# Kernel tuning notes

Measured on AMD Instinct MI355X. Metric: run time of the kernel, lower is better.

## Reference

```python
import jax, jax.numpy as jnp
import numpy as np

SEQ, IN, H = 65536, 64, 128


def setup_inputs() -> dict:
    key = jax.random.key(0)
    ks = jax.random.split(key, 7)
    s_i, s_h = 1.0 / np.sqrt(IN), 1.0 / np.sqrt(H)
    return {
        "input_seq": jax.random.normal(ks[0], (SEQ, IN), jnp.float32),
        "W_ih": jax.random.normal(ks[1], (4 * H, IN), jnp.float32) * s_i,
        "W_hh": jax.random.normal(ks[2], (4 * H, H), jnp.float32) * s_h,
        "b_ih": jax.random.normal(ks[3], (4 * H,), jnp.float32) * s_h,
        "b_hh": jax.random.normal(ks[4], (4 * H,), jnp.float32) * s_h,
        "W_lin": jax.random.normal(ks[5], (1, H), jnp.float32) * s_h,
        "b_lin": jax.random.normal(ks[6], (1,), jnp.float32) * s_h,
    }


def reference(input_seq, W_ih, W_hh, b_ih, b_hh, W_lin, b_lin):
    # Precompute input contributions to all gates: [SEQ, 4H]
    x_gates = input_seq @ W_ih.T + b_ih + b_hh

    def step(carry, xg):
        h, c = carry
        gates = xg + h @ W_hh.T  # [4H]
        i, f, g, o = jnp.split(gates, 4)
        i = jax.nn.sigmoid(i)
        f = jax.nn.sigmoid(f)
        g = jnp.tanh(g)
        o = jax.nn.sigmoid(o)
        c = f * c + i * g
        h = o * jnp.tanh(c)
        return (h, c), None

    h0 = jnp.zeros((H,), input_seq.dtype)
    c0 = jnp.zeros((H,), input_seq.dtype)
    (hT, _), _ = jax.lax.scan(step, (h0, c0), x_gates)
    # outputs[-1] == sigmoid(linear(h_T)); shape [1]
    return jax.nn.sigmoid(hT @ W_lin.T + b_lin)
```

## Files before the change

### kernel.cpp

```cpp
#include <hip/hip_runtime.h>

#define SEQ 65536
#define IN_DIM 64
#define H 128
#define G4 512

typedef _Float16 half_t;
typedef half_t half2_t __attribute__((ext_vector_type(2)));
typedef half_t half8_t __attribute__((ext_vector_type(8)));

__device__ __forceinline__ float fast_rcp(float x) { return __builtin_amdgcn_rcpf(x); }

__device__ __forceinline__ float sigmoid_f(float x) {
    x = fminf(fmaxf(x, -30.f), 30.f);
    return fast_rcp(1.f + __expf(-x));
}

__device__ __forceinline__ float tanh_f(float x) {
    x = fminf(fmaxf(x, -15.f), 15.f);
    float e = __expf(2.f * x);
    return (e - 1.f) * fast_rcp(e + 1.f);
}

#if __has_builtin(__builtin_amdgcn_fdot2)
__device__ __forceinline__ float dot2(half2_t a, half2_t b, float c) {
    return __builtin_amdgcn_fdot2(a, b, c, false);
}
#else
__device__ __forceinline__ float dot2(half2_t a, half2_t b, float c) {
    return c + (float)a[0] * (float)b[0] + (float)a[1] * (float)b[1];
}
#endif

__device__ __forceinline__ half2_t pick2(half8_t v, int i0) {
    half2_t r; r[0] = v[i0]; r[1] = v[i0 + 1]; return r;
}

__device__ __forceinline__ half8_t cvt8(const float* p) {
    float4 a = *(const float4*)p;
    float4 b = *(const float4*)(p + 4);
    half8_t r;
    r[0] = (half_t)a.x; r[1] = (half_t)a.y; r[2] = (half_t)a.z; r[3] = (half_t)a.w;
    r[4] = (half_t)b.x; r[5] = (half_t)b.y; r[6] = (half_t)b.z; r[7] = (half_t)b.w;
    return r;
}

#if __has_builtin(__builtin_amdgcn_mov_dpp)
__device__ __forceinline__ float qx1(float x) {
    return __int_as_float(__builtin_amdgcn_mov_dpp(__float_as_int(x), 0xB1, 0xF, 0xF, true));
}
__device__ __forceinline__ float qx2(float x) {
    return __int_as_float(__builtin_amdgcn_mov_dpp(__float_as_int(x), 0x4E, 0xF, 0xF, true));
}
#else
__device__ __forceinline__ float qx1(float x) { return __shfl_xor(x, 1, 4); }
__device__ __forceinline__ float qx2(float x) { return __shfl_xor(x, 2, 4); }
#endif

__global__ __launch_bounds__(256) void xg_gemm(
    const float* __restrict__ x, const float* __restrict__ Wih,
    const float* __restrict__ bih, const float* __restrict__ bhh,
    float* __restrict__ xg)
{
    long long gid = (long long)blockIdx.x * 256 + threadIdx.x;
    int s = (int)(gid >> 9);
    int rr = (int)(gid & 511);
    int j = rr >> 2, g = rr & 3;
    int row = g * H + j;
    const float* xr = x + (long long)s * IN_DIM;
    const float* wr = Wih + (long long)row * IN_DIM;
    float a0 = 0.f, a1 = 0.f, a2 = 0.f, a3 = 0.f;
#pragma unroll
    for (int k = 0; k < IN_DIM; k += 4) {
        float4 iv = *(const float4*)(xr + k);
        float4 wv = *(const float4*)(wr + k);
        a0 += wv.x * iv.x; a1 += wv.y * iv.y;
        a2 += wv.z * iv.z; a3 += wv.w * iv.w;
    }
    xg[gid] = (a0 + a1) + (a2 + a3) + bih[row] + bhh[row];
}

__global__ __launch_bounds__(256, 1) void lstm_scan(
    const float* __restrict__ Whh, const float* __restrict__ Wlin,
    const float* __restrict__ blin, const float* __restrict__ xg,
    float* __restrict__ out)
{
    __shared__ __align__(16) half_t shbuf[2][H];
    const int tid = threadIdx.x;
    const int ql = tid & 3;
    const int j0 = (tid >> 2) * 2;
    const int c0 = ql * 32;
    const int jrow = j0 + (ql & 1);

#define LOADW(P, ROW)                                                     \
    half8_t P##0 = cvt8(Whh + (size_t)(ROW) * H + c0 + 0),                \
            P##1 = cvt8(Whh + (size_t)(ROW) * H + c0 + 8),                \
            P##2 = cvt8(Whh + (size_t)(ROW) * H + c0 + 16),               \
            P##3 = cvt8(Whh + (size_t)(ROW) * H + c0 + 24);
    LOADW(wi0, j0)           LOADW(wi1, j0 + 1)
    LOADW(wf0, 128 + j0)     LOADW(wf1, 129 + j0)
    LOADW(wg0, 256 + j0)     LOADW(wg1, 257 + j0)
    LOADW(wo0, 384 + j0)     LOADW(wo1, 385 + j0)
#undef LOADW
#define PIN(A, B, C, D) asm volatile("" : "+v"(A), "+v"(B), "+v"(C), "+v"(D))
    PIN(wi00, wi01, wi02, wi03); PIN(wi10, wi11, wi12, wi13);
    PIN(wf00, wf01, wf02, wf03); PIN(wf10, wf11, wf12, wf13);
    PIN(wg00, wg01, wg02, wg03); PIN(wg10, wg11, wg12, wg13);
    PIN(wo00, wo01, wo02, wo03); PIN(wo10, wo11, wo12, wo13);
#undef PIN

    float c = 0.f;
    float4 xgv = {0.f, 0.f, 0.f, 0.f};
    if (ql < 2) xgv = *(const float4*)(xg + (size_t)jrow * 4);
    if (tid < H) shbuf[0][tid] = (half_t)0.f;
    __syncthreads();

#define DOT8(ACC, WV, HV)                                                 \
    ACC = dot2(pick2(WV, 0), pick2(HV, 0), ACC);                          \
    ACC = dot2(pick2(WV, 2), pick2(HV, 2), ACC);                          \
    ACC = dot2(pick2(WV, 4), pick2(HV, 4), ACC);                          \
    ACC = dot2(pick2(WV, 6), pick2(HV, 6), ACC);
#define DOTROW(ACC, P)                                                    \
    DOT8(ACC, P##0, h0) DOT8(ACC, P##1, h1)                               \
    DOT8(ACC, P##2, h2) DOT8(ACC, P##3, h3)
#define QRED(X) X += qx1(X); X += qx2(X);

#define STEP(RB, WB, T)                                                   \
    {                                                                     \
        const half8_t* hp = (const half8_t*)&shbuf[RB][c0];               \
        half8_t h0 = hp[0], h1 = hp[1], h2 = hp[2], h3 = hp[3];           \
        int tn = (T) + 1; if (tn > SEQ - 1) tn = SEQ - 1;                 \
        float4 xg_n = {0.f, 0.f, 0.f, 0.f};                               \
        if (ql < 2)                                                       \
            xg_n = *(const float4*)(xg + (size_t)tn * G4 + jrow * 4);     \
        float ai0 = 0.f, ai1 = 0.f, af0 = 0.f, af1 = 0.f;                 \
        float ag0 = 0.f, ag1 = 0.f, ao0 = 0.f, ao1 = 0.f;                 \
        DOTROW(ai0, wi0) DOTROW(ai1, wi1)                                 \
        DOTROW(af0, wf0) DOTROW(af1, wf1)                                 \
        DOTROW(ag0, wg0) DOTROW(ag1, wg1)                                 \
        DOTROW(ao0, wo0) DOTROW(ao1, wo1)                                 \
        QRED(ai0) QRED(ai1) QRED(af0) QRED(af1)                           \
        QRED(ag0) QRED(ag1) QRED(ao0) QRED(ao1)                           \
        if (ql < 2) {                                                     \
            float si = ql ? ai1 : ai0, sf = ql ? af1 : af0;               \
            float sg = ql ? ag1 : ag0, so = ql ? ao1 : ao0;               \
            float gi = sigmoid_f(si + xgv.x);                             \
            float gf = sigmoid_f(sf + xgv.y);                             \
            float gg = tanh_f(sg + xgv.z);                                \
            float go = sigmoid_f(so + xgv.w);                             \
            c = gf * c + gi * gg;                                         \
            shbuf[WB][jrow] = (half_t)(go * tanh_f(c));                   \
        }                                                                 \
        __syncthreads();                                                  \
        xgv = xg_n;                                                       \
    }

    for (int t = 0; t < SEQ; t += 2) {
        STEP(0, 1, t)
        STEP(1, 0, t + 1)
    }
#undef STEP
#undef QRED
#undef DOTROW
#undef DOT8

    if (tid < 64) {
        float p = (float)shbuf[0][tid] * Wlin[tid] +
                  (float)shbuf[0][tid + 64] * Wlin[tid + 64];
#pragma unroll
        for (int off = 32; off > 0; off >>= 1) p += __shfl_down(p, off);
        if (tid == 0) out[0] = sigmoid_f(p + blin[0]);
    }
}

__global__ __launch_bounds__(512, 2) void lstm_scan_fb(
    const float* __restrict__ x, const float* __restrict__ Wih,
    const float* __restrict__ Whh, const float* __restrict__ bih,
    const float* __restrict__ bhh, const float* __restrict__ Wlin,
    const float* __restrict__ blin, float* __restrict__ out)
{
    __shared__ __align__(16) half_t sh_h[H];
    __shared__ __align__(16) float  sh_g[G4];
    const int row = threadIdx.x;
    const float* wrow = Whh + (long long)row * H;

    half8_t w0  = cvt8(wrow + 0),   w1  = cvt8(wrow + 8);
    half8_t w2  = cvt8(wrow + 16),  w3  = cvt8(wrow + 24);
    half8_t w4  = cvt8(wrow + 32),  w5  = cvt8(wrow + 40);
    half8_t w6  = cvt8(wrow + 48),  w7  = cvt8(wrow + 56);
    half8_t w8  = cvt8(wrow + 64),  w9  = cvt8(wrow + 72);
    half8_t w10 = cvt8(wrow + 80),  w11 = cvt8(wrow + 88);
    half8_t w12 = cvt8(wrow + 96),  w13 = cvt8(wrow + 104);
    half8_t w14 = cvt8(wrow + 112), w15 = cvt8(wrow + 120);

    const float bsum = bih[row] + bhh[row];
    float c = 0.f;
    if (row < H) sh_h[row] = (half_t)0.f;

    float xg_cur;
    {
        float a = bsum;
        const float* wir = Wih + (long long)row * IN_DIM;
#pragma unroll
        for (int k = 0; k < IN_DIM; k += 4) {
            float4 iv = *(const float4*)(x + k);
            float4 wv = *(const float4*)(wir + k);
            a += wv.x * iv.x + wv.y * iv.y + wv.z * iv.z + wv.w * iv.w;
        }
        xg_cur = a;
    }
    const bool is_g = (row >= 2 * H) && (row < 3 * H);
    __syncthreads();

    const half8_t* hch = (const half8_t*)sh_h;

    for (int t = 0; t < SEQ; ++t) {
        float xg_nxt = 0.f;
        if (t + 1 < SEQ) {
            const float* xr = x + (size_t)(t + 1) * IN_DIM;
            const float* wir = Wih + (long long)row * IN_DIM;
            float a = bsum;
#pragma unroll
            for (int k = 0; k < IN_DIM; k += 4) {
                float4 iv = *(const float4*)(xr + k);
                float4 wv = *(const float4*)(wir + k);
                a += wv.x * iv.x + wv.y * iv.y + wv.z * iv.z + wv.w * iv.w;
            }
            xg_nxt = a;
        }
        float a0 = 0.f, a1 = 0.f, a2 = 0.f, a3 = 0.f;
#define DOTC(WV, CI)                                                     \
        {   half8_t hv = hch[CI];                                        \
            a0 = dot2(pick2(WV, 0), pick2(hv, 0), a0);                   \
            a1 = dot2(pick2(WV, 2), pick2(hv, 2), a1);                   \
            a2 = dot2(pick2(WV, 4), pick2(hv, 4), a2);                   \
            a3 = dot2(pick2(WV, 6), pick2(hv, 6), a3); }
        DOTC(w0, 0)  DOTC(w1, 1)  DOTC(w2, 2)   DOTC(w3, 3)
        DOTC(w4, 4)  DOTC(w5, 5)  DOTC(w6, 6)   DOTC(w7, 7)
        DOTC(w8, 8)  DOTC(w9, 9)  DOTC(w10, 10) DOTC(w11, 11)
        DOTC(w12, 12) DOTC(w13, 13) DOTC(w14, 14) DOTC(w15, 15)
#undef DOTC
        float pre = xg_cur + ((a0 + a1) + (a2 + a3));
        float gv = is_g ? tanh_f(pre) : sigmoid_f(pre);
        sh_g[row] = gv;
        __syncthreads();
        if (row >= 3 * H) {
            int j = row - 3 * H;
            float ig = sh_g[j];
            float fg = sh_g[H + j];
            float gg = sh_g[2 * H + j];
            c = fg * c + ig * gg;
            sh_h[j] = (half_t)(gv * tanh_f(c));
        }
        __syncthreads();
        xg_cur = xg_nxt;
    }

    if (row < 64) {
        float p = (float)sh_h[row] * Wlin[row] +
                  (float)sh_h[row + 64] * Wlin[row + 64];
#pragma unroll
        for (int off = 32; off > 0; off >>= 1) p += __shfl_down(p, off);
        if (row == 0) out[0] = sigmoid_f(p + blin[0]);
    }
}

extern "C" void kernel_launch(void* const* d_in, const int* in_sizes, int n_in,
                              void* d_out, int out_size, void* d_ws, size_t ws_size,
                              hipStream_t stream)
{
    const float* x    = (const float*)d_in[0];
    const float* Wih  = (const float*)d_in[1];
    const float* Whh  = (const float*)d_in[2];
    const float* bih  = (const float*)d_in[3];
    const float* bhh  = (const float*)d_in[4];
    const float* Wlin = (const float*)d_in[5];
    const float* blin = (const float*)d_in[6];
    float* out = (float*)d_out;

    const size_t need = (size_t)SEQ * G4 * sizeof(float);
    if (ws_size >= need) {
        float* xg = (float*)d_ws;
        xg_gemm<<<(SEQ * G4) / 256, 256, 0, stream>>>(x, Wih, bih, bhh, xg);
        lstm_scan<<<1, 256, 0, stream>>>(Whh, Wlin, blin, xg, out);
    } else {
        lstm_scan_fb<<<1, 512, 0, stream>>>(x, Wih, Whh, bih, bhh, Wlin,
                                            blin, out);
    }
}
```

Baseline: 33.12 ms.

## Spread gate activations across quad lanes and exchange via DPP in LSTM scan

Each lane of a 4-lane quad now computes the activation for one gate type (i, f, g, o) for two hidden units, and the four results are exchanged with DPP permutes, so all quad lanes do activation work instead of only half of them. tanh is computed as 2*sigmoid(2x)-1 so every lane runs the same instruction sequence. The xg buffer goes back to its natural row layout, loaded as float2 and prefetched two steps ahead. The __syncthreads is replaced with an explicit lgkmcnt wait, s_barrier and a sched_barrier. The aim is a shorter serial critical path per timestep, at the cost of extra permutes and reliance on hand-placed barrier semantics.

```diff
diff --git a/kernel.cpp b/kernel.cpp
--- a/kernel.cpp
+++ b/kernel.cpp
@@ -14,12 +14,6 @@
 __device__ __forceinline__ float sigmoid_f(float x) {
     x = fminf(fmaxf(x, -30.f), 30.f);
     return fast_rcp(1.f + __expf(-x));
-}
-
-__device__ __forceinline__ float tanh_f(float x) {
-    x = fminf(fmaxf(x, -15.f), 15.f);
-    float e = __expf(2.f * x);
-    return (e - 1.f) * fast_rcp(e + 1.f);
 }
 
 #if __has_builtin(__builtin_amdgcn_fdot2)
@@ -45,17 +39,14 @@
     return r;
 }
 
-#if __has_builtin(__builtin_amdgcn_mov_dpp)
-__device__ __forceinline__ float qx1(float x) {
-    return __int_as_float(__builtin_amdgcn_mov_dpp(__float_as_int(x), 0xB1, 0xF, 0xF, true));
-}
-__device__ __forceinline__ float qx2(float x) {
-    return __int_as_float(__builtin_amdgcn_mov_dpp(__float_as_int(x), 0x4E, 0xF, 0xF, true));
-}
-#else
-__device__ __forceinline__ float qx1(float x) { return __shfl_xor(x, 1, 4); }
-__device__ __forceinline__ float qx2(float x) { return __shfl_xor(x, 2, 4); }
-#endif
+template <int CTRL>
+__device__ __forceinline__ float qperm(float x) {
+    return __int_as_float(
+        __builtin_amdgcn_mov_dpp(__float_as_int(x), CTRL, 0xF, 0xF, true));
+}
+#define qx1(x)  qperm<0xB1>(x)
+#define qx2(x)  qperm<0x4E>(x)
+#define qrev(x) qperm<0x1B>(x)
 
 __global__ __launch_bounds__(256) void xg_gemm(
     const float* __restrict__ x, const float* __restrict__ Wih,
@@ -64,11 +55,9 @@
 {
     long long gid = (long long)blockIdx.x * 256 + threadIdx.x;
     int s = (int)(gid >> 9);
-    int rr = (int)(gid & 511);
-    int j = rr >> 2, g = rr & 3;
-    int row = g * H + j;
+    int r = (int)(gid & 511);
     const float* xr = x + (long long)s * IN_DIM;
-    const float* wr = Wih + (long long)row * IN_DIM;
+    const float* wr = Wih + (long long)r * IN_DIM;
     float a0 = 0.f, a1 = 0.f, a2 = 0.f, a3 = 0.f;
 #pragma unroll
     for (int k = 0; k < IN_DIM; k += 4) {
@@ -77,7 +66,7 @@
         a0 += wv.x * iv.x; a1 += wv.y * iv.y;
         a2 += wv.z * iv.z; a3 += wv.w * iv.w;
     }
-    xg[gid] = (a0 + a1) + (a2 + a3) + bih[row] + bhh[row];
+    xg[gid] = (a0 + a1) + (a2 + a3) + bih[r] + bhh[r];
 }
 
 __global__ __launch_bounds__(256, 1) void lstm_scan(
@@ -90,7 +79,6 @@
     const int ql = tid & 3;
     const int j0 = (tid >> 2) * 2;
     const int c0 = ql * 32;
-    const int jrow = j0 + (ql & 1);
 
 #define LOADW(P, ROW)                                                     \
     half8_t P##0 = cvt8(Whh + (size_t)(ROW) * H + c0 + 0),                \
@@ -109,9 +97,14 @@
     PIN(wo00, wo01, wo02, wo03); PIN(wo10, wo11, wo12, wo13);
 #undef PIN
 
+    const bool isg = (ql == 2);
+    const bool l0  = (ql == 0);
+    const float* xgbase = xg + ql * H + j0;
     float c = 0.f;
-    float4 xgv = {0.f, 0.f, 0.f, 0.f};
-    if (ql < 2) xgv = *(const float4*)(xg + (size_t)jrow * 4);
+
+    float2 xg_c = *(const float2*)(xgbase + (size_t)0 * G4);
+    float2 xg_n = *(const float2*)(xgbase + (size_t)1 * G4);
+
     if (tid < H) shbuf[0][tid] = (half_t)0.f;
     __syncthreads();
 
@@ -129,10 +122,8 @@
     {                                                                     \
         const half8_t* hp = (const half8_t*)&shbuf[RB][c0];               \
         half8_t h0 = hp[0], h1 = hp[1], h2 = hp[2], h3 = hp[3];           \
-        int tn = (T) + 1; if (tn > SEQ - 1) tn = SEQ - 1;                 \
-        float4 xg_n = {0.f, 0.f, 0.f, 0.f};                               \
-        if (ql < 2)                                                       \
-            xg_n = *(const float4*)(xg + (size_t)tn * G4 + jrow * 4);     \
+        int tp = (T) + 2; if (tp > SEQ - 1) tp = SEQ - 1;                 \
+        float2 xg_p = *(const float2*)(xgbase + (size_t)tp * G4);         \
         float ai0 = 0.f, ai1 = 0.f, af0 = 0.f, af1 = 0.f;                 \
         float ag0 = 0.f, ag1 = 0.f, ao0 = 0.f, ao1 = 0.f;                 \
         DOTROW(ai0, wi0) DOTROW(ai1, wi1)                                 \
@@ -141,18 +132,33 @@
         DOTROW(ao0, wo0) DOTROW(ao1, wo1)                                 \
         QRED(ai0) QRED(ai1) QRED(af0) QRED(af1)                           \
         QRED(ag0) QRED(ag1) QRED(ao0) QRED(ao1)                           \
-        if (ql < 2) {                                                     \
-            float si = ql ? ai1 : ai0, sf = ql ? af1 : af0;               \
-            float sg = ql ? ag1 : ag0, so = ql ? ao1 : ao0;               \
-            float gi = sigmoid_f(si + xgv.x);                             \
-            float gf = sigmoid_f(sf + xgv.y);                             \
-            float gg = tanh_f(sg + xgv.z);                                \
-            float go = sigmoid_f(so + xgv.w);                             \
-            c = gf * c + gi * gg;                                         \
-            shbuf[WB][jrow] = (half_t)(go * tanh_f(c));                   \
-        }                                                                 \
-        __syncthreads();                                                  \
-        xgv = xg_n;                                                       \
+                         \
+        float sa = ai0, sb = ai1;                                         \
+        if (ql == 1) { sa = af0; sb = af1; }                              \
+        if (ql == 2) { sa = ag0; sb = ag1; }                              \
+        if (ql == 3) { sa = ao0; sb = ao1; }                              \
+        float xa = sa + xg_c.x, xb = sb + xg_c.y;                         \
+        float ua = isg ? xa + xa : xa;                                    \
+        float ub = isg ? xb + xb : xb;                                    \
+        float ra = sigmoid_f(ua), rb = sigmoid_f(ub);                     \
+        float gva = isg ? ra + ra - 1.f : ra;        \
+        float gvb = isg ? rb + rb - 1.f : rb;                             \
+          \
+        float fA = qx1(gva), iB = qx1(gvb);                               \
+        float gA = qx2(gva), oB = qx2(gvb);                               \
+        float oA = qrev(gva), gB = qrev(gvb);                             \
+        float ii = l0 ? gva : iB;                                         \
+        float ff = l0 ? fA  : gvb;                                        \
+        float gg = l0 ? gA  : gB;                                         \
+        float oo = l0 ? oA  : oB;                                         \
+        c = ff * c + ii * gg;                                             \
+        float th = 2.f * sigmoid_f(c + c) - 1.f;                          \
+        float hh = oo * th;                                               \
+        if (ql < 2) shbuf[WB][j0 + ql] = (half_t)hh;                      \
+        asm volatile("s_waitcnt lgkmcnt(0)" ::: "memory");                \
+        __builtin_amdgcn_s_barrier();                                     \
+        __builtin_amdgcn_sched_barrier(0);                                \
+        xg_c = xg_n; xg_n = xg_p;                                         \
     }
 
     for (int t = 0; t < SEQ; t += 2) {
@@ -241,7 +247,13 @@
         DOTC(w12, 12) DOTC(w13, 13) DOTC(w14, 14) DOTC(w15, 15)
 #undef DOTC
         float pre = xg_cur + ((a0 + a1) + (a2 + a3));
-        float gv = is_g ? tanh_f(pre) : sigmoid_f(pre);
+        float gv;
+        if (is_g) {
+            float s = sigmoid_f(pre + pre);
+            gv = s + s - 1.f;
+        } else {
+            gv = sigmoid_f(pre);
+        }
         sh_g[row] = gv;
         __syncthreads();
         if (row >= 3 * H) {
@@ -250,7 +262,8 @@
             float fg = sh_g[H + j];
             float gg = sh_g[2 * H + j];
             c = fg * c + ig * gg;
-            sh_h[j] = (half_t)(gv * tanh_f(c));
+            float s = sigmoid_f(c + c);
+            sh_h[j] = (half_t)(gv * (s + s - 1.f));
         }
         __syncthreads();
         xg_cur = xg_nxt;
```

Result: faster. 32.30 ms (-2.5%).
